# Performance work log

Hardware: AMD Instinct MI355X
Metric: run time of the kernel (lower is better)

## Reference

```python
import jax, jax.numpy as jnp
import numpy as np

DIM = 1024
DEPTH = 6
HEADS = 16
MLP_DIM = 4096
EPS = 1e-5


def setup_inputs() -> dict:
    key = jax.random.key(0)
    ks = jax.random.split(key, 8)
    d, L, f = DIM, DEPTH, MLP_DIM
    s = lambda fan_in: 1.0 / np.sqrt(fan_in)
    inp = {
        "x": jax.random.normal(ks[0], (4, 1024, d), dtype=jnp.float32),
        "ln1_w": jnp.ones((L, d), jnp.float32),
        "ln1_b": jnp.zeros((L, d), jnp.float32),
        "qkv_w": jax.random.normal(ks[1], (L, d, 3 * d), jnp.float32) * s(d),
        "qkv_b": jnp.zeros((L, 3 * d), jnp.float32),
        "proj_w": jax.random.normal(ks[2], (L, d, d), jnp.float32) * s(d),
        "proj_b": jnp.zeros((L, d), jnp.float32),
        "ln2_w": jnp.ones((L, d), jnp.float32),
        "ln2_b": jnp.zeros((L, d), jnp.float32),
        "mlp_w1": jax.random.normal(ks[3], (L, d, f), jnp.float32) * s(d),
        "mlp_b1": jax.random.normal(ks[4], (L, f), jnp.float32) * 1e-6,
        "mlp_w2": jax.random.normal(ks[5], (L, f, d), jnp.float32) * s(f),
        "mlp_b2": jax.random.normal(ks[6], (L, d), jnp.float32) * 1e-6,
    }
    return inp


def _layer_norm(x, w, b):
    mu = jnp.mean(x, axis=-1, keepdims=True)
    var = jnp.mean(jnp.square(x - mu), axis=-1, keepdims=True)
    return (x - mu) * jax.lax.rsqrt(var + EPS) * w + b


def _block(x, ln1_w, ln1_b, qkv_w, qkv_b, proj_w, proj_b,
           ln2_w, ln2_b, mlp_w1, mlp_b1, mlp_w2, mlp_b2):
    b, n, d = x.shape
    h = HEADS
    hd = d // h
    scale = d ** (-0.5)  # note: original scales by dim**-0.5, not head_dim**-0.5
    # attention sublayer (pre-LN + residual)
    y = _layer_norm(x, ln1_w, ln1_b)
    qkv = y @ qkv_w + qkv_b                      # [b, n, 3d]
    qkv = qkv.reshape(b, n, 3, h, hd)            # matches 'b n (qkv h d)'
    q, k, v = (jnp.moveaxis(qkv[:, :, i], 1, 2) for i in range(3))  # [b, h, n, hd]
    dots = jnp.einsum('bhid,bhjd->bhij', q, k) * scale
    attn = jax.nn.softmax(dots, axis=-1)
    out = jnp.einsum('bhij,bhjd->bhid', attn, v)
    out = jnp.moveaxis(out, 1, 2).reshape(b, n, d)
    x = x + out @ proj_w + proj_b
    # MLP sublayer (pre-LN + residual)
    y = _layer_norm(x, ln2_w, ln2_b)
    y = jax.nn.gelu(y @ mlp_w1 + mlp_b1, approximate=False)
    x = x + y @ mlp_w2 + mlp_b2
    return x


def reference(x, ln1_w, ln1_b, qkv_w, qkv_b, proj_w, proj_b,
              ln2_w, ln2_b, mlp_w1, mlp_b1, mlp_w2, mlp_b2):
    for l in range(DEPTH):
        x = _block(x, ln1_w[l], ln1_b[l], qkv_w[l], qkv_b[l],
                   proj_w[l], proj_b[l], ln2_w[l], ln2_b[l],
                   mlp_w1[l], mlp_b1[l], mlp_w2[l], mlp_b2[l])
    return x
```

## Files before the change

### kernel.cpp

```cpp
#include <hip/hip_runtime.h>

typedef __attribute__((ext_vector_type(8))) short short8;
typedef __attribute__((ext_vector_type(4))) float floatx4;

#define DIM   1024
#define SEQ   1024
#define BATCH 4
#define NHEAD 16
#define HDIM  64
#define MLPD  4096
#define DEPTH 6
#define MTOK  (BATCH*SEQ)

__device__ __forceinline__ unsigned short f2bf(float f) {
    union { float f; unsigned u; } v; v.f = f;
    unsigned r = v.u + 0x7fffu + ((v.u >> 16) & 1u);
    return (unsigned short)(r >> 16);
}

__device__ __forceinline__ void gld16(const void* g, void* l) {
    __builtin_amdgcn_global_load_lds(
        (const __attribute__((address_space(1))) unsigned int*)g,
        (__attribute__((address_space(3))) unsigned int*)l, 16, 0, 0);
}

__global__ __launch_bounds__(256) void ln_kernel(
    const float* __restrict__ x, const float* __restrict__ w,
    const float* __restrict__ b, unsigned short* __restrict__ y)
{
    __shared__ float red[8];
    const int row = blockIdx.x;
    const int t = threadIdx.x;
    const float4 v = ((const float4*)(x + (size_t)row * DIM))[t];
    float s = v.x + v.y + v.z + v.w;
#pragma unroll
    for (int m = 1; m < 64; m <<= 1) s += __shfl_xor(s, m);
    if ((t & 63) == 0) red[t >> 6] = s;
    __syncthreads();
    const float mu = (red[0] + red[1] + red[2] + red[3]) * (1.0f / DIM);
    const float d0 = v.x - mu, d1 = v.y - mu, d2 = v.z - mu, d3 = v.w - mu;
    float q = d0 * d0 + d1 * d1 + d2 * d2 + d3 * d3;
#pragma unroll
    for (int m = 1; m < 64; m <<= 1) q += __shfl_xor(q, m);
    if ((t & 63) == 0) red[4 + (t >> 6)] = q;
    __syncthreads();
    const float var = (red[4] + red[5] + red[6] + red[7]) * (1.0f / DIM);
    const float rs = rsqrtf(var + 1e-5f);
    const float4 wv = ((const float4*)w)[t];
    const float4 bv = ((const float4*)b)[t];
    ushort4 o;
    o.x = f2bf(d0 * rs * wv.x + bv.x);
    o.y = f2bf(d1 * rs * wv.y + bv.y);
    o.z = f2bf(d2 * rs * wv.z + bv.z);
    o.w = f2bf(d3 * rs * wv.w + bv.w);
    ((ushort4*)(y + (size_t)row * DIM))[t] = o;
}

__global__ __launch_bounds__(256) void wtrans_kernel(
    const float* __restrict__ W, unsigned short* __restrict__ Wt, int K, int N)
{
    __shared__ float tile[64][65];
    const int n0 = blockIdx.x * 64, k0 = blockIdx.y * 64;
    const int t = threadIdx.x;
#pragma unroll
    for (int p = t; p < 1024; p += 256) {
        const int k = p >> 4, nq = (p & 15) * 4;
        const float4 v = *(const float4*)&W[(size_t)(k0 + k) * N + n0 + nq];
        tile[k][nq + 0] = v.x; tile[k][nq + 1] = v.y;
        tile[k][nq + 2] = v.z; tile[k][nq + 3] = v.w;
    }
    __syncthreads();
#pragma unroll
    for (int p = t; p < 1024; p += 256) {
        const int n = p >> 4, kq = (p & 15) * 4;
        ushort4 o;
        o.x = f2bf(tile[kq + 0][n]); o.y = f2bf(tile[kq + 1][n]);
        o.z = f2bf(tile[kq + 2][n]); o.w = f2bf(tile[kq + 3][n]);
        *(ushort4*)&Wt[(size_t)(n0 + n) * K + k0 + kq] = o;
    }
}

template <int MODE>
__global__ __launch_bounds__(256) void gemm_pipe(
    const unsigned short* __restrict__ A, const unsigned short* __restrict__ Bt,
    const float* __restrict__ bias, void* __restrict__ Cout,
    int M, int K, int N)
{
    __shared__ __align__(16) unsigned short Al[2 * 128 * 32];
    __shared__ __align__(16) unsigned short Bl[2 * 128 * 32];

    const int bm = blockIdx.y * 128, bn = blockIdx.x * 128;
    const int tid = threadIdx.x;
    const int lane = tid & 63, wid = tid >> 6;
    const int lm = lane & 15, quad = lane >> 4;
    const int wm = (wid >> 1) * 64, wn = (wid & 1) * 64;

    floatx4 acc[4][4] = {};

    const unsigned short* gA = A + (size_t)(bm + wid * 32 + (lane >> 2)) * K + (lane & 3) * 8;
    const unsigned short* gB = Bt + (size_t)(bn + wid * 32 + (lane >> 2)) * K + (lane & 3) * 8;
    const int wof = wid * 1024;

    gld16(gA, &Al[wof]);
    gld16(gA + (size_t)16 * K, &Al[wof + 512]);
    gld16(gB, &Bl[wof]);
    gld16(gB + (size_t)16 * K, &Bl[wof + 512]);

    const int nk = K >> 5;
    for (int i = 0; i < nk; i++) {
        __syncthreads();
        const int cur = (i & 1) * 4096;
        if (i + 1 < nk) {
            const int nxt = ((i + 1) & 1) * 4096;
            const int kt = (i + 1) * 32;
            gld16(gA + kt, &Al[nxt + wof]);
            gld16(gA + (size_t)16 * K + kt, &Al[nxt + wof + 512]);
            gld16(gB + kt, &Bl[nxt + wof]);
            gld16(gB + (size_t)16 * K + kt, &Bl[nxt + wof + 512]);
        }
        short8 af[4], bf[4];
#pragma unroll
        for (int t = 0; t < 4; t++)
            af[t] = *(const short8*)&Al[cur + (wm + t * 16 + lm) * 32 + quad * 8];
#pragma unroll
        for (int t = 0; t < 4; t++)
            bf[t] = *(const short8*)&Bl[cur + (wn + t * 16 + lm) * 32 + quad * 8];
#pragma unroll
        for (int t = 0; t < 4; t++)
#pragma unroll
            for (int j = 0; j < 4; j++)
                acc[t][j] = __builtin_amdgcn_mfma_f32_16x16x32_bf16(
                    af[t], bf[j], acc[t][j], 0, 0, 0);
    }

#pragma unroll
    for (int i = 0; i < 4; i++) {
        const int row = bm + wm + i * 16 + quad * 4;
#pragma unroll
        for (int j = 0; j < 4; j++) {
            const int col = bn + wn + j * 16 + lm;
            const float bb = bias[col];
#pragma unroll
            for (int r = 0; r < 4; r++) {
                float v = acc[i][j][r] + bb;
                const size_t idx = (size_t)(row + r) * N + col;
                if constexpr (MODE == 0) {
                    ((unsigned short*)Cout)[idx] = f2bf(v);
                } else if constexpr (MODE == 1) {
                    const float g = 0.5f * v * (1.0f + erff(v * 0.70710678118654752f));
                    ((unsigned short*)Cout)[idx] = f2bf(g);
                } else {
                    ((float*)Cout)[idx] += v;
                }
            }
        }
    }
}

__global__ __launch_bounds__(256) void vtrans_kernel(
    const unsigned short* __restrict__ qkv, unsigned short* __restrict__ Vt)
{
    __shared__ unsigned short tile[64][65];
    const int bh = blockIdx.x, nt = blockIdx.y;
    const int b = bh >> 4, h = bh & 15;
    const int t = threadIdx.x;
#pragma unroll
    for (int p = t; p < 4096; p += 256) {
        const int n = p >> 6, c = p & 63;
        tile[n][c] = qkv[(size_t)(b * SEQ + nt * 64 + n) * (3 * DIM) + 2 * DIM + h * HDIM + c];
    }
    __syncthreads();
#pragma unroll
    for (int p = t; p < 4096; p += 256) {
        const int hd = p >> 6, n = p & 63;
        Vt[((size_t)bh * HDIM + hd) * SEQ + nt * 64 + n] = tile[n][hd];
    }
}

__global__ __launch_bounds__(256) void attn_kernel(
    const unsigned short* __restrict__ qkv, const unsigned short* __restrict__ Vt,
    unsigned short* __restrict__ O)
{
    __shared__ __align__(16) unsigned short P[2][4][32 * 72];
    const int bh = blockIdx.x;
    const int b = bh >> 4, h = bh & 15;
    const int tid = threadIdx.x, lane = tid & 63, wid = tid >> 6;
    const int lm = lane & 15, quad = lane >> 4;
    const int q0 = (blockIdx.y * 4 + wid) * 32;

    const unsigned short* Qbase = qkv + (size_t)(b * SEQ) * (3 * DIM) + h * HDIM;
    const unsigned short* Kbase = Qbase + DIM;
    const unsigned short* Vbase = Vt + (size_t)bh * HDIM * SEQ;

    short8 aq[2][2];
#pragma unroll
    for (int qt = 0; qt < 2; qt++)
#pragma unroll
        for (int t = 0; t < 2; t++)
            aq[qt][t] = *(const short8*)&Qbase[(size_t)(q0 + qt * 16 + lm) * (3 * DIM) + t * 32 + quad * 8];

    short8 ones;
#pragma unroll
    for (int t = 0; t < 8; t++) ones[t] = (short)0x3F80;

    floatx4 o[2][4] = {};
    floatx4 sacc[2] = {};
    const float scale = 0.03125f;
    const float M = 3.0f;

    for (int i = 0; i < SEQ / 64; i++) {
        const int kt = i * 64;
        short8 bk[4][2];
#pragma unroll
        for (int s = 0; s < 4; s++)
#pragma unroll
            for (int t = 0; t < 2; t++)
                bk[s][t] = *(const short8*)&Kbase[(size_t)(kt + s * 16 + lm) * (3 * DIM) + t * 32 + quad * 8];
        short8 bv[4][2];
#pragma unroll
        for (int ht = 0; ht < 4; ht++)
#pragma unroll
            for (int kh = 0; kh < 2; kh++)
                bv[ht][kh] = *(const short8*)&Vbase[(size_t)(ht * 16 + lm) * SEQ + kt + kh * 32 + quad * 8];

        unsigned short* Pw = P[i & 1][wid];
#pragma unroll
        for (int qt = 0; qt < 2; qt++)
#pragma unroll
            for (int s = 0; s < 4; s++) {
                floatx4 sv = {};
                sv = __builtin_amdgcn_mfma_f32_16x16x32_bf16(aq[qt][0], bk[s][0], sv, 0, 0, 0);
                sv = __builtin_amdgcn_mfma_f32_16x16x32_bf16(aq[qt][1], bk[s][1], sv, 0, 0, 0);
#pragma unroll
                for (int r = 0; r < 4; r++)
                    Pw[(qt * 16 + quad * 4 + r) * 72 + s * 16 + lm] =
                        f2bf(__expf(fmaf(sv[r], scale, -M)));
            }
        short8 pa[2][2];
#pragma unroll
        for (int qt = 0; qt < 2; qt++)
#pragma unroll
            for (int kh = 0; kh < 2; kh++)
                pa[qt][kh] = *(const short8*)&Pw[(qt * 16 + lm) * 72 + kh * 32 + quad * 8];
#pragma unroll
        for (int qt = 0; qt < 2; qt++) {
            sacc[qt] = __builtin_amdgcn_mfma_f32_16x16x32_bf16(pa[qt][0], ones, sacc[qt], 0, 0, 0);
            sacc[qt] = __builtin_amdgcn_mfma_f32_16x16x32_bf16(pa[qt][1], ones, sacc[qt], 0, 0, 0);
        }
#pragma unroll
        for (int qt = 0; qt < 2; qt++)
#pragma unroll
            for (int ht = 0; ht < 4; ht++) {
                o[qt][ht] = __builtin_amdgcn_mfma_f32_16x16x32_bf16(pa[qt][0], bv[ht][0], o[qt][ht], 0, 0, 0);
                o[qt][ht] = __builtin_amdgcn_mfma_f32_16x16x32_bf16(pa[qt][1], bv[ht][1], o[qt][ht], 0, 0, 0);
            }
    }

#pragma unroll
    for (int qt = 0; qt < 2; qt++)
#pragma unroll
        for (int r = 0; r < 4; r++) {
            const float inv = 1.0f / sacc[qt][r];
            const int qrow = q0 + qt * 16 + quad * 4 + r;
            const size_t orow = (size_t)(b * SEQ + qrow) * DIM + h * HDIM;
#pragma unroll
            for (int ti = 0; ti < 4; ti++)
                O[orow + ti * 16 + lm] = f2bf(o[qt][ti][r] * inv);
        }
}

extern "C" void kernel_launch(void* const* d_in, const int* in_sizes, int n_in,
                              void* d_out, int out_size, void* d_ws, size_t ws_size,
                              hipStream_t stream)
{
    (void)in_sizes; (void)n_in; (void)out_size; (void)ws_size;
    const float* x      = (const float*)d_in[0];
    const float* ln1_w  = (const float*)d_in[1];
    const float* ln1_b  = (const float*)d_in[2];
    const float* qkv_w  = (const float*)d_in[3];
    const float* qkv_b  = (const float*)d_in[4];
    const float* proj_w = (const float*)d_in[5];
    const float* proj_b = (const float*)d_in[6];
    const float* ln2_w  = (const float*)d_in[7];
    const float* ln2_b  = (const float*)d_in[8];
    const float* mlp_w1 = (const float*)d_in[9];
    const float* mlp_b1 = (const float*)d_in[10];
    const float* mlp_w2 = (const float*)d_in[11];
    const float* mlp_b2 = (const float*)d_in[12];

    char* p = (char*)d_ws;
    float* xbuf = (float*)p;                    p += (size_t)MTOK * DIM * 4;
    unsigned short* y = (unsigned short*)p;     p += (size_t)MTOK * DIM * 2;
    unsigned short* big = (unsigned short*)p;   p += (size_t)MTOK * MLPD * 2;
    unsigned short* Vt = (unsigned short*)p;    p += (size_t)MTOK * DIM * 2;
    unsigned short* attno = (unsigned short*)p; p += (size_t)MTOK * DIM * 2;
    unsigned short* qkvT = (unsigned short*)p;  p += (size_t)DIM * 3 * DIM * 2;
    unsigned short* projT = (unsigned short*)p; p += (size_t)DIM * DIM * 2;
    unsigned short* mlp1T = (unsigned short*)p; p += (size_t)DIM * MLPD * 2;
    unsigned short* mlp2T = (unsigned short*)p; p += (size_t)MLPD * DIM * 2;

    hipMemcpyAsync(xbuf, x, (size_t)MTOK * DIM * 4, hipMemcpyDeviceToDevice, stream);

    for (int l = 0; l < DEPTH; l++) {
        wtrans_kernel<<<dim3(3 * DIM / 64, DIM / 64), 256, 0, stream>>>(
            qkv_w + (size_t)l * DIM * 3 * DIM, qkvT, DIM, 3 * DIM);
        wtrans_kernel<<<dim3(DIM / 64, DIM / 64), 256, 0, stream>>>(
            proj_w + (size_t)l * DIM * DIM, projT, DIM, DIM);
        wtrans_kernel<<<dim3(MLPD / 64, DIM / 64), 256, 0, stream>>>(
            mlp_w1 + (size_t)l * DIM * MLPD, mlp1T, DIM, MLPD);
        wtrans_kernel<<<dim3(DIM / 64, MLPD / 64), 256, 0, stream>>>(
            mlp_w2 + (size_t)l * MLPD * DIM, mlp2T, MLPD, DIM);

        ln_kernel<<<MTOK, 256, 0, stream>>>(xbuf, ln1_w + l * DIM, ln1_b + l * DIM, y);
        gemm_pipe<0><<<dim3(3 * DIM / 128, MTOK / 128), 256, 0, stream>>>(
            y, qkvT, qkv_b + (size_t)l * 3 * DIM, big, MTOK, DIM, 3 * DIM);
        vtrans_kernel<<<dim3(64, 16), 256, 0, stream>>>(big, Vt);
        attn_kernel<<<dim3(64, 8), 256, 0, stream>>>(big, Vt, attno);
        gemm_pipe<2><<<dim3(DIM / 128, MTOK / 128), 256, 0, stream>>>(
            attno, projT, proj_b + (size_t)l * DIM, xbuf, MTOK, DIM, DIM);
        ln_kernel<<<MTOK, 256, 0, stream>>>(xbuf, ln2_w + l * DIM, ln2_b + l * DIM, y);
        gemm_pipe<1><<<dim3(MLPD / 128, MTOK / 128), 256, 0, stream>>>(
            y, mlp1T, mlp_b1 + (size_t)l * MLPD, big, MTOK, DIM, MLPD);
        gemm_pipe<2><<<dim3(DIM / 128, MTOK / 128), 256, 0, stream>>>(
            big, mlp2T, mlp_b2 + (size_t)l * DIM, xbuf, MTOK, MLPD, DIM);
    }
    hipMemcpyAsync(d_out, xbuf, (size_t)MTOK * DIM * 4, hipMemcpyDeviceToDevice, stream);
}
```

Before: 2.190 ms.

## Replace GEMM with 256x256-tile 8-wave pipelined kernel and split-K MLP2

Replaces the 128x128 double-buffered GEMM with a 256x256 tile, 512-thread kernel. It uses a K=64 step, XOR-swizzled LDS layout, staggered async global-to-LDS loads interleaved with MFMA phases, and s_setprio around the compute. The second MLP GEMM is split along K into four slices that accumulate with atomicAdd, to restore parallelism on its small output grid. The larger tiles cut global traffic per FLOP. The costs are larger LDS use (128KB), fewer blocks for the small GEMMs, atomic contention, and nondeterministic summation order.

```diff
diff --git a/kernel.cpp b/kernel.cpp
--- a/kernel.cpp
+++ b/kernel.cpp
@@ -81,80 +81,161 @@
 }
 
 template <int MODE>
-__global__ __launch_bounds__(256) void gemm_pipe(
+__global__ __launch_bounds__(512, 2) void gemm8(
     const unsigned short* __restrict__ A, const unsigned short* __restrict__ Bt,
     const float* __restrict__ bias, void* __restrict__ Cout,
-    int M, int K, int N)
-{
-    __shared__ __align__(16) unsigned short Al[2 * 128 * 32];
-    __shared__ __align__(16) unsigned short Bl[2 * 128 * 32];
-
-    const int bm = blockIdx.y * 128, bn = blockIdx.x * 128;
-    const int tid = threadIdx.x;
+    int M, int ldk, int Keff, int N)
+{
+    (void)M;
+    __shared__ __align__(16) unsigned short Lds[65536];
+    unsigned short* const LA = Lds;
+    unsigned short* const LB = Lds + 32768;
+
+    const int bm = blockIdx.y * 256, bn = blockIdx.x * 256;
+    const int kz = blockIdx.z;
+    const int tid  = threadIdx.x;
     const int lane = tid & 63, wid = tid >> 6;
     const int lm = lane & 15, quad = lane >> 4;
-    const int wm = (wid >> 1) * 64, wn = (wid & 1) * 64;
-
-    floatx4 acc[4][4] = {};
-
-    const unsigned short* gA = A + (size_t)(bm + wid * 32 + (lane >> 2)) * K + (lane & 3) * 8;
-    const unsigned short* gB = Bt + (size_t)(bn + wid * 32 + (lane >> 2)) * K + (lane & 3) * 8;
-    const int wof = wid * 1024;
-
-    gld16(gA, &Al[wof]);
-    gld16(gA + (size_t)16 * K, &Al[wof + 512]);
-    gld16(gB, &Bl[wof]);
-    gld16(gB + (size_t)16 * K, &Bl[wof + 512]);
-
-    const int nk = K >> 5;
-    for (int i = 0; i < nk; i++) {
-        __syncthreads();
-        const int cur = (i & 1) * 4096;
-        if (i + 1 < nk) {
-            const int nxt = ((i + 1) & 1) * 4096;
-            const int kt = (i + 1) * 32;
-            gld16(gA + kt, &Al[nxt + wof]);
-            gld16(gA + (size_t)16 * K + kt, &Al[nxt + wof + 512]);
-            gld16(gB + kt, &Bl[nxt + wof]);
-            gld16(gB + (size_t)16 * K + kt, &Bl[nxt + wof + 512]);
-        }
-        short8 af[4], bf[4];
-#pragma unroll
-        for (int t = 0; t < 4; t++)
-            af[t] = *(const short8*)&Al[cur + (wm + t * 16 + lm) * 32 + quad * 8];
-#pragma unroll
-        for (int t = 0; t < 4; t++)
-            bf[t] = *(const short8*)&Bl[cur + (wn + t * 16 + lm) * 32 + quad * 8];
-#pragma unroll
-        for (int t = 0; t < 4; t++)
-#pragma unroll
-            for (int j = 0; j < 4; j++)
-                acc[t][j] = __builtin_amdgcn_mfma_f32_16x16x32_bf16(
-                    af[t], bf[j], acc[t][j], 0, 0, 0);
-    }
-
-#pragma unroll
-    for (int i = 0; i < 4; i++) {
-        const int row = bm + wm + i * 16 + quad * 4;
-#pragma unroll
-        for (int j = 0; j < 4; j++) {
-            const int col = bn + wn + j * 16 + lm;
-            const float bb = bias[col];
-#pragma unroll
-            for (int r = 0; r < 4; r++) {
-                float v = acc[i][j][r] + bb;
-                const size_t idx = (size_t)(row + r) * N + col;
-                if constexpr (MODE == 0) {
-                    ((unsigned short*)Cout)[idx] = f2bf(v);
-                } else if constexpr (MODE == 1) {
-                    const float g = 0.5f * v * (1.0f + erff(v * 0.70710678118654752f));
-                    ((unsigned short*)Cout)[idx] = f2bf(g);
-                } else {
-                    ((float*)Cout)[idx] += v;
+    const int wrow = wid >> 2, wcol = wid & 3;
+
+    const int l8    = lane >> 3;
+    const int chunk = (((lane & 7) ^ l8) << 3);
+    const int reg0  = wid * 2, reg1 = reg0 + 1;
+    const size_t hstep = (size_t)128 * ldk;
+
+    const unsigned short* gA0 = A  + (size_t)kz * Keff + (size_t)(bm + reg0 * 8 + l8) * ldk + chunk;
+    const unsigned short* gA1 = A  + (size_t)kz * Keff + (size_t)(bm + reg1 * 8 + l8) * ldk + chunk;
+    const unsigned short* gB0 = Bt + (size_t)kz * Keff + (size_t)(bn + reg0 * 8 + l8) * ldk + chunk;
+    const unsigned short* gB1 = Bt + (size_t)kz * Keff + (size_t)(bn + reg1 * 8 + l8) * ldk + chunk;
+
+    auto stA = [&](int s, int h, int t) {
+        gld16(gA0 + h * hstep + t * 64, LA + s * 16384 + h * 8192 + reg0 * 512);
+        gld16(gA1 + h * hstep + t * 64, LA + s * 16384 + h * 8192 + reg1 * 512);
+    };
+    auto stB = [&](int s, int h, int t) {
+        gld16(gB0 + h * hstep + t * 64, LB + s * 16384 + h * 8192 + reg0 * 512);
+        gld16(gB1 + h * hstep + t * 64, LB + s * 16384 + h * 8192 + reg1 * 512);
+    };
+
+    floatx4 acc[8][4] = {};
+    short8 bfr[2][4];
+
+    const int NT = Keff >> 6;
+
+    stA(0, 0, 0); stA(0, 1, 0); stB(0, 0, 0); stB(0, 1, 0);
+    stA(1, 0, 1); stB(1, 0, 1); stB(1, 1, 1);
+    asm volatile("s_waitcnt vmcnt(6)" ::: "memory");
+    __builtin_amdgcn_sched_barrier(0);
+    __builtin_amdgcn_s_barrier();
+
+    const int arow0 = wrow * 64 + lm;
+    const int brow0 = wcol * 64 + lm;
+    const char* const lAc = (const char*)LA;
+    const char* const lBc = (const char*)LB;
+
+#define RD(base, sOff, row, cb) \
+    (*(const short8*)((base) + (sOff) + (row) * 128 + ((cb) ^ (((row) & 7) << 4))))
+
+    for (int t = 0; t < NT; ++t) {
+        const int s = t & 1, s2 = s ^ 1;
+        const int sOff = s * 32768;
+        short8 af[4];
+
+#pragma unroll
+        for (int ti = 0; ti < 4; ti++) af[ti]     = RD(lAc, sOff, arow0 + ti * 16, quad * 16);
+#pragma unroll
+        for (int ni = 0; ni < 4; ni++) bfr[0][ni] = RD(lBc, sOff, brow0 + ni * 16, quad * 16);
+        if (t + 1 < NT) stA(s2, 1, t + 1);
+        __builtin_amdgcn_s_barrier();
+        asm volatile("s_waitcnt lgkmcnt(0)" ::: "memory");
+        __builtin_amdgcn_sched_barrier(0);
+        __builtin_amdgcn_s_setprio(1);
+#pragma unroll
+        for (int ti = 0; ti < 4; ti++)
+#pragma unroll
+            for (int ni = 0; ni < 4; ni++)
+                acc[ti][ni] = __builtin_amdgcn_mfma_f32_16x16x32_bf16(af[ti], bfr[0][ni], acc[ti][ni], 0, 0, 0);
+        __builtin_amdgcn_s_setprio(0);
+        __builtin_amdgcn_s_barrier();
+
+#pragma unroll
+        for (int ti = 0; ti < 4; ti++) af[ti]     = RD(lAc, sOff, arow0 + ti * 16, 64 + quad * 16);
+#pragma unroll
+        for (int ni = 0; ni < 4; ni++) bfr[1][ni] = RD(lBc, sOff, brow0 + ni * 16, 64 + quad * 16);
+        __builtin_amdgcn_s_barrier();
+        asm volatile("s_waitcnt lgkmcnt(0)" ::: "memory");
+        __builtin_amdgcn_sched_barrier(0);
+        __builtin_amdgcn_s_setprio(1);
+#pragma unroll
+        for (int ti = 0; ti < 4; ti++)
+#pragma unroll
+            for (int ni = 0; ni < 4; ni++)
+                acc[ti][ni] = __builtin_amdgcn_mfma_f32_16x16x32_bf16(af[ti], bfr[1][ni], acc[ti][ni], 0, 0, 0);
+        __builtin_amdgcn_s_setprio(0);
+        __builtin_amdgcn_s_barrier();
+
+#pragma unroll
+        for (int ti = 0; ti < 4; ti++) af[ti] = RD(lAc, sOff, 128 + arow0 + ti * 16, quad * 16);
+        if (t + 2 < NT) { stA(s, 0, t + 2); stB(s, 0, t + 2); }
+        __builtin_amdgcn_s_barrier();
+        asm volatile("s_waitcnt lgkmcnt(0)" ::: "memory");
+        __builtin_amdgcn_sched_barrier(0);
+        __builtin_amdgcn_s_setprio(1);
+#pragma unroll
+        for (int ti = 0; ti < 4; ti++)
+#pragma unroll
+            for (int ni = 0; ni < 4; ni++)
+                acc[4 + ti][ni] = __builtin_amdgcn_mfma_f32_16x16x32_bf16(af[ti], bfr[0][ni], acc[4 + ti][ni], 0, 0, 0);
+        __builtin_amdgcn_s_setprio(0);
+        __builtin_amdgcn_s_barrier();
+
+#pragma unroll
+        for (int ti = 0; ti < 4; ti++) af[ti] = RD(lAc, sOff, 128 + arow0 + ti * 16, 64 + quad * 16);
+        if (t + 2 < NT) stB(s, 1, t + 2);
+        __builtin_amdgcn_s_barrier();
+        asm volatile("s_waitcnt lgkmcnt(0)" ::: "memory");
+        __builtin_amdgcn_sched_barrier(0);
+        __builtin_amdgcn_s_setprio(1);
+#pragma unroll
+        for (int ti = 0; ti < 4; ti++)
+#pragma unroll
+            for (int ni = 0; ni < 4; ni++)
+                acc[4 + ti][ni] = __builtin_amdgcn_mfma_f32_16x16x32_bf16(af[ti], bfr[1][ni], acc[4 + ti][ni], 0, 0, 0);
+        __builtin_amdgcn_s_setprio(0);
+        if (t + 2 < NT) { asm volatile("s_waitcnt vmcnt(6)" ::: "memory"); }
+        else            { asm volatile("s_waitcnt vmcnt(0)" ::: "memory"); }
+        __builtin_amdgcn_sched_barrier(0);
+        __builtin_amdgcn_s_barrier();
+    }
+#undef RD
+
+#pragma unroll
+    for (int st = 0; st < 2; st++)
+#pragma unroll
+        for (int ti = 0; ti < 4; ti++) {
+            const int row = bm + st * 128 + wrow * 64 + ti * 16 + quad * 4;
+#pragma unroll
+            for (int ni = 0; ni < 4; ni++) {
+                const int col = bn + wcol * 64 + ni * 16 + lm;
+                const float bb = (MODE == 3 && kz != 0) ? 0.0f : bias[col];
+                const floatx4 a = acc[st * 4 + ti][ni];
+#pragma unroll
+                for (int r = 0; r < 4; r++) {
+                    float v = a[r] + bb;
+                    const size_t idx = (size_t)(row + r) * N + col;
+                    if constexpr (MODE == 0) {
+                        ((unsigned short*)Cout)[idx] = f2bf(v);
+                    } else if constexpr (MODE == 1) {
+                        const float g = 0.5f * v * (1.0f + erff(v * 0.70710678118654752f));
+                        ((unsigned short*)Cout)[idx] = f2bf(g);
+                    } else if constexpr (MODE == 2) {
+                        ((float*)Cout)[idx] += v;
+                    } else {
+                        atomicAdd(&((float*)Cout)[idx], v);
+                    }
                 }
             }
         }
-    }
 }
 
 __global__ __launch_bounds__(256) void vtrans_kernel(
@@ -312,17 +393,17 @@
             mlp_w2 + (size_t)l * MLPD * DIM, mlp2T, MLPD, DIM);
 
         ln_kernel<<<MTOK, 256, 0, stream>>>(xbuf, ln1_w + l * DIM, ln1_b + l * DIM, y);
-        gemm_pipe<0><<<dim3(3 * DIM / 128, MTOK / 128), 256, 0, stream>>>(
-            y, qkvT, qkv_b + (size_t)l * 3 * DIM, big, MTOK, DIM, 3 * DIM);
+        gemm8<0><<<dim3(3 * DIM / 256, MTOK / 256), 512, 0, stream>>>(
+            y, qkvT, qkv_b + (size_t)l * 3 * DIM, big, MTOK, DIM, DIM, 3 * DIM);
         vtrans_kernel<<<dim3(64, 16), 256, 0, stream>>>(big, Vt);
         attn_kernel<<<dim3(64, 8), 256, 0, stream>>>(big, Vt, attno);
-        gemm_pipe<2><<<dim3(DIM / 128, MTOK / 128), 256, 0, stream>>>(
-            attno, projT, proj_b + (size_t)l * DIM, xbuf, MTOK, DIM, DIM);
+        gemm8<2><<<dim3(DIM / 256, MTOK / 256), 512, 0, stream>>>(
+            attno, projT, proj_b + (size_t)l * DIM, xbuf, MTOK, DIM, DIM, DIM);
         ln_kernel<<<MTOK, 256, 0, stream>>>(xbuf, ln2_w + l * DIM, ln2_b + l * DIM, y);
-        gemm_pipe<1><<<dim3(MLPD / 128, MTOK / 128), 256, 0, stream>>>(
-            y, mlp1T, mlp_b1 + (size_t)l * MLPD, big, MTOK, DIM, MLPD);
-        gemm_pipe<2><<<dim3(DIM / 128, MTOK / 128), 256, 0, stream>>>(
-            big, mlp2T, mlp_b2 + (size_t)l * DIM, xbuf, MTOK, MLPD, DIM);
+        gemm8<1><<<dim3(MLPD / 256, MTOK / 256), 512, 0, stream>>>(
+            y, mlp1T, mlp_b1 + (size_t)l * MLPD, big, MTOK, DIM, DIM, MLPD);
+        gemm8<3><<<dim3(DIM / 256, MTOK / 256, 4), 512, 0, stream>>>(
+            big, mlp2T, mlp_b2 + (size_t)l * DIM, xbuf, MTOK, MLPD, MLPD / 4, DIM);
     }
     hipMemcpyAsync(d_out, xbuf, (size_t)MTOK * DIM * 4, hipMemcpyDeviceToDevice, stream);
 }
```

After: 2.185 ms. No clear change (-0.2%).
